# Optimization experiments

Measured on AMD Instinct MI355X. Metric: run time of the kernel, lower is better.

Reference implementation:

```python
import jax, jax.numpy as jnp
import numpy as np

NUM_GRAPHS = 128
EPS = 1e-5  # torch BatchNorm1d default eps


def setup_inputs() -> dict:
    key = jax.random.key(0)
    ks = jax.random.split(key, 24)
    N, E, NHE = 50000, 800000, 50000
    NODE_RAW, HEDGE_RAW, H, HH, HOUT = 92, 40, 128, 128, 256
    s = 0.05
    inp = {
        "x": jax.random.normal(ks[0], (N, NODE_RAW), jnp.float32),
        "hedge_attrs": jax.random.normal(ks[1], (NHE, HEDGE_RAW), jnp.float32),
        "inter_relations_index": jax.random.randint(ks[2], (3, E), 0, N, jnp.int64),
        "batch": jax.random.randint(ks[3], (N,), 0, NUM_GRAPHS, jnp.int64),
        "num_nodes": N,
        # embed: Linear(92, h_dim)
        "embed_w": jax.random.normal(ks[4], (NODE_RAW, H), jnp.float32) * s,
        "embed_b": jax.random.normal(ks[5], (H,), jnp.float32) * s,
        # bembed: Linear(hedge_dim, hidden_hedge_dim)
        "bembed_w": jax.random.normal(ks[6], (HEDGE_RAW, HH), jnp.float32) * s,
        "bembed_b": jax.random.normal(ks[7], (HH,), jnp.float32) * s,
        # conv.lin_full_presplit: Linear(2H+HH, 2H)
        "lin_w": jax.random.normal(ks[8], (2 * H + HH, 2 * H), jnp.float32) * s,
        "lin_b": jax.random.normal(ks[9], (2 * H,), jnp.float32) * s,
        "bn1_g": jnp.ones((2 * H,), jnp.float32),
        "bn1_b": jnp.zeros((2 * H,), jnp.float32),
        "bn2_g": jnp.ones((H,), jnp.float32),
        "bn2_b": jnp.zeros((H,), jnp.float32),
        # learnable temperature of SoftmaxAggregation (init 1.0)
        "aggr_t": jnp.ones((), jnp.float32),
        "l1_w": jax.random.normal(ks[10], (H, HOUT), jnp.float32) * s,
        "l1_b": jax.random.normal(ks[11], (HOUT,), jnp.float32) * s,
        "out_w": jax.random.normal(ks[12], (HOUT, 1), jnp.float32) * s,
        "out_b": jax.random.normal(ks[13], (1,), jnp.float32) * s,
    }
    return inp


def _batchnorm(z, g, b):
    mu = z.mean(axis=0)
    var = z.var(axis=0)  # biased, matching torch training-mode normalization
    return (z - mu) * jax.lax.rsqrt(var + EPS) * g + b


def reference(x, hedge_attrs, inter_relations_index, batch, num_nodes,
              embed_w, embed_b, bembed_w, bembed_b, lin_w, lin_b,
              bn1_g, bn1_b, bn2_g, bn2_b, aggr_t, l1_w, l1_b, out_w, out_b):
    idx0 = inter_relations_index[0]
    idx1 = inter_relations_index[1]
    connect_feats = hedge_attrs @ bembed_w + bembed_b          # [NHE, HH]
    h = x @ embed_w + embed_b                                   # [N, H]

    # --- CHGInterConv ---
    origin = h[idx0]                                            # [E, H]
    connect = connect_feats[idx1]                               # [E, HH]
    remote = h[idx0]                                            # faithful to source (uses idx0)
    z = jnp.concatenate([origin, connect, remote], axis=1)      # [E, 2H+HH]
    z = z @ lin_w + lin_b                                       # [E, 2H]
    z = _batchnorm(z, bn1_g, bn1_b)
    z_f, z_c = jnp.split(z, 2, axis=-1)
    msg = jax.nn.sigmoid(z_f) * jax.nn.softplus(z_c)            # [E, H]

    # learned SoftmaxAggregation: per-node, per-channel segment softmax of t*msg
    alpha = msg * aggr_t
    m = jax.ops.segment_max(alpha, idx0, num_segments=num_nodes)
    m = jnp.where(jnp.isfinite(m), m, 0.0)                      # empty segments
    e = jnp.exp(alpha - m[idx0])
    denom = jax.ops.segment_sum(e, idx0, num_segments=num_nodes)
    w = e / (denom[idx0] + 1e-16)
    out = jax.ops.segment_sum(msg * w, idx0, num_segments=num_nodes)  # [N, H]

    out = _batchnorm(out, bn2_g, bn2_b)
    h = jax.nn.softplus(out + h)                                # residual + softplus

    # --- global mean pool over graphs ---
    counts = jax.ops.segment_sum(jnp.ones((num_nodes,), h.dtype), batch,
                                 num_segments=NUM_GRAPHS)
    pooled = jax.ops.segment_sum(h, batch, num_segments=NUM_GRAPHS)
    pooled = pooled / jnp.maximum(counts, 1.0)[:, None]         # [G, H]

    g = jax.nn.softplus(pooled @ l1_w + l1_b)                   # [G, HOUT]
    return g @ out_w + out_b                                    # [G, 1]
```

## Files before the change

### kernel.cpp

```cpp
#include <hip/hip_runtime.h>
#include <hip/hip_bf16.h>


#define EPS_BN 1e-5f
#define LOG2E 1.4426950408889634f
#define LN2   0.6931471805599453f

#define BIN_SH 8
#define BIN_CHUNK 4096

typedef __attribute__((ext_vector_type(8))) short bf16x8;
typedef __attribute__((ext_vector_type(4))) float f32x4;
typedef __attribute__((ext_vector_type(2))) float f32x2;

__device__ __forceinline__ float fexp2(float x) {
#if __has_builtin(__builtin_amdgcn_exp2f)
    return __builtin_amdgcn_exp2f(x);
#else
    return __expf(x * LN2);
#endif
}
__device__ __forceinline__ float flog2(float x) {
#if __has_builtin(__builtin_amdgcn_logf)
    return __builtin_amdgcn_logf(x);
#else
    return __logf(x) * LOG2E;
#endif
}
__device__ __forceinline__ float softplus_fast(float x) {
    return LN2 * flog2(1.f + fexp2(x * LOG2E));
}

__device__ __forceinline__ f32x2 pk_fma2(f32x2 a, f32x2 b, f32x2 c) {
#if __has_builtin(__builtin_elementwise_fma)
    return __builtin_elementwise_fma(a, b, c);
#else
    return (f32x2){fmaf(a.x, b.x, c.x), fmaf(a.y, b.y, c.y)};
#endif
}

__device__ __forceinline__ unsigned short f2bf(float f) {
    unsigned u = __float_as_uint(f);
    unsigned r = (u + 0x7fffu + ((u >> 16) & 1u)) >> 16;
    return (unsigned short)r;
}
__device__ __forceinline__ float bflo(unsigned u) { return __uint_as_float(u << 16); }
__device__ __forceinline__ float bfhi(unsigned u) { return __uint_as_float(u & 0xffff0000u); }
__device__ __forceinline__ float bfu16(unsigned short v) { return __uint_as_float(((unsigned)v) << 16); }
__device__ __forceinline__ unsigned pack2bf(float x, float y) {
    return (unsigned)f2bf(x) | ((unsigned)f2bf(y) << 16);
}

#if __has_builtin(__builtin_amdgcn_cvt_pk_f32_fp8) && __has_builtin(__builtin_amdgcn_cvt_pk_fp8_f32)
#define HW_FP8 1
#else
#define HW_FP8 0
#endif

__device__ __forceinline__ unsigned char f2fp8(float f) {
#if HW_FP8
    int r = __builtin_amdgcn_cvt_pk_fp8_f32(f, f, 0, false);
    return (unsigned char)(r & 0xff);
#else
    unsigned u = __float_as_uint(f);
    unsigned s = (u >> 24) & 0x80u;
    float af = fabsf(f);
    if (!(af >= 0.015625f)) {
        int m = (int)rintf(af * 512.f);
        if (m > 7) m = 7;
        return (unsigned char)(s | (unsigned)m);
    }
    if (af > 448.f) return (unsigned char)(s | 0x7e);
    unsigned au = __float_as_uint(af);
    unsigned r = au + 0x7ffffu + ((au >> 20) & 1u);
    int e8 = (int)(r >> 23) - 120;
    unsigned m = (r >> 20) & 7u;
    if (e8 > 15 || (e8 == 15 && m == 7)) return (unsigned char)(s | 0x7e);
    return (unsigned char)(s | ((unsigned)e8 << 3) | m);
#endif
}

__device__ __forceinline__ void fp8pair(unsigned p, f32x2& lo, f32x2& hi) {
#if HW_FP8
    lo = __builtin_amdgcn_cvt_pk_f32_fp8((int)p, false);
    hi = __builtin_amdgcn_cvt_pk_f32_fp8((int)p, true);
#else
    auto dec = [](unsigned byte) -> float {
        unsigned s = (byte & 0x80u) << 24;
        unsigned em = byte & 0x7fu;
        float nrm = __uint_as_float(s | ((em << 20) + 0x3C000000u));
        float sub = __uint_as_float(s | 0x3F800000u) * (float)em * 0.001953125f;
        return (em >= 8) ? nrm : sub;
    };
    lo = (f32x2){dec(p & 0xff), dec((p >> 8) & 0xff)};
    hi = (f32x2){dec((p >> 16) & 0xff), dec(p >> 24)};
#endif
}

__device__ __forceinline__ int perm256(int j) {
    return (j < 128) ? ((j >> 1) * 4 + (j & 1)) : (((j - 128) >> 1) * 4 + 2 + (j & 1));
}

__global__ __launch_bounds__(256) void k_prepw(const float* __restrict__ ew, const float* __restrict__ bw,
                                               const float* __restrict__ lw,
                                               unsigned short* __restrict__ embB, unsigned short* __restrict__ bembB,
                                               unsigned short* __restrict__ waB, unsigned short* __restrict__ wcB) {
    int i = blockIdx.x * 256 + threadIdx.x;
    if (i >= 81920) return;
    unsigned short* dst;
    int f, NKC, CT, mode;
    if (i < 12288)      { dst = embB;  f = i;         NKC = 3; CT = 2; mode = 0; }
    else if (i < 20480) { dst = bembB; f = i - 12288; NKC = 2; CT = 2; mode = 1; }
    else if (i < 53248) { dst = waB;   f = i - 20480; NKC = 4; CT = 4; mode = 2; }
    else                { dst = wcB;   f = i - 53248; NKC = 4; CT = 4; mode = 3; }
    int j = f & 7, l = (f >> 3) & 63;
    int r2 = f >> 9;
    int c = r2 % CT;
    int r3 = r2 / CT;
    int kc = r3 % NKC, w = r3 / NKC;
    int k = kc * 32 + ((l >> 4) & 3) * 8 + j;
    int n = (w * CT + c) * 16 + (l & 15);
    float v;
    if (mode == 0)      v = (k < 92) ? ew[k * 128 + n] : 0.f;
    else if (mode == 1) v = (k < 40) ? bw[k * 128 + n] : 0.f;
    else if (mode == 2) v = lw[k * 256 + n] + lw[(k + 256) * 256 + n];
    else                v = lw[(k + 128) * 256 + n];
    dst[f] = f2bf(v);
}

template<int KIN, int NKC1, int OMODE2>
__global__ __launch_bounds__(256) void mfma_fused(
    const float* __restrict__ in, const unsigned short* __restrict__ B1, const float* __restrict__ bias1,
    const unsigned short* __restrict__ B2, const float* __restrict__ bias2,
    unsigned short* __restrict__ hout, void* __restrict__ out2, int M,
    const int* __restrict__ aux_idx, int* __restrict__ aux_hist, int aux_cnt)
{
    const int r0 = blockIdx.x * 32;
    const int t = threadIdx.x;
    const int w = t >> 6;
    const int l = t & 63;
    const int m = l & 15, q = l >> 4;

    if (aux_idx) {
        const int T = gridDim.x * 256;
        for (int i = blockIdx.x * 256 + t; i < aux_cnt; i += T)
            atomicAdd(&aux_hist[aux_idx[i]], 1);
    }

    __shared__ __align__(16) unsigned short als[32 * NKC1 * 32];
    __shared__ __align__(16) unsigned short hls[32 * 136];

    const int KP = NKC1 * 32;
    for (int i = t; i < 32 * KP; i += 256) {
        int r = i / KP, k = i - r * KP;
        int gr = r0 + r;
        float v = (gr < M && k < KIN) ? in[(size_t)gr * KIN + k] : 0.f;
        int idx = (((r >> 4) * NKC1 + (k >> 5)) * 64 + ((k >> 3) & 3) * 16 + (r & 15)) * 8 + (k & 7);
        als[idx] = f2bf(v);
    }
    bf16x8 b1[NKC1][2];
    const bf16x8* B1f = (const bf16x8*)B1;
#pragma unroll
    for (int kc = 0; kc < NKC1; kc++)
#pragma unroll
        for (int c = 0; c < 2; c++)
            b1[kc][c] = B1f[((w * NKC1 + kc) * 2 + c) * 64 + l];
    __syncthreads();

    f32x4 acc1[2][2];
#pragma unroll
    for (int c = 0; c < 2; c++) { acc1[c][0] = (f32x4){0.f,0.f,0.f,0.f}; acc1[c][1] = (f32x4){0.f,0.f,0.f,0.f}; }
    const bf16x8* af = (const bf16x8*)als;
#pragma unroll
    for (int kc = 0; kc < NKC1; kc++) {
        bf16x8 a0 = af[kc * 64 + l];
        bf16x8 a1 = af[(NKC1 + kc) * 64 + l];
#pragma unroll
        for (int c = 0; c < 2; c++) {
            acc1[c][0] = __builtin_amdgcn_mfma_f32_16x16x32_bf16(a0, b1[kc][c], acc1[c][0], 0, 0, 0);
            acc1[c][1] = __builtin_amdgcn_mfma_f32_16x16x32_bf16(a1, b1[kc][c], acc1[c][1], 0, 0, 0);
        }
    }
#pragma unroll
    for (int c = 0; c < 2; c++) {
        int n1 = (w * 2 + c) * 16 + m;
        float bv = bias1[n1];
#pragma unroll
        for (int hh = 0; hh < 2; hh++) {
#pragma unroll
            for (int r = 0; r < 4; r++) {
                int row = hh * 16 + q * 4 + r;
                float val = acc1[c][hh][r] + bv;
                unsigned short bf = f2bf(val);
                hls[row * 136 + n1] = bf;
                if (OMODE2 == 1 && r0 + row < M) hout[(size_t)(r0 + row) * 128 + n1] = bf;
            }
        }
    }
    __syncthreads();

    bf16x8 b2[4][4];
    const bf16x8* B2f = (const bf16x8*)B2;
#pragma unroll
    for (int kc = 0; kc < 4; kc++)
#pragma unroll
        for (int c = 0; c < 4; c++)
            b2[kc][c] = B2f[((w * 4 + kc) * 4 + c) * 64 + l];

    f32x4 acc2[4][2];
#pragma unroll
    for (int c = 0; c < 4; c++) { acc2[c][0] = (f32x4){0.f,0.f,0.f,0.f}; acc2[c][1] = (f32x4){0.f,0.f,0.f,0.f}; }
#pragma unroll
    for (int kc = 0; kc < 4; kc++) {
        bf16x8 a0 = *(const bf16x8*)(hls + m * 136 + kc * 32 + q * 8);
        bf16x8 a1 = *(const bf16x8*)(hls + (m + 16) * 136 + kc * 32 + q * 8);
#pragma unroll
        for (int c = 0; c < 4; c++) {
            acc2[c][0] = __builtin_amdgcn_mfma_f32_16x16x32_bf16(a0, b2[kc][c], acc2[c][0], 0, 0, 0);
            acc2[c][1] = __builtin_amdgcn_mfma_f32_16x16x32_bf16(a1, b2[kc][c], acc2[c][1], 0, 0, 0);
        }
    }
#pragma unroll
    for (int c = 0; c < 4; c++) {
        int n = (w * 4 + c) * 16 + m;
        float bv = bias2 ? bias2[n] : 0.f;
        int pj = perm256(n);
#pragma unroll
        for (int hh = 0; hh < 2; hh++) {
#pragma unroll
            for (int r = 0; r < 4; r++) {
                int row = r0 + hh * 16 + q * 4 + r;
                if (row < M) {
                    float val = acc2[c][hh][r] + bv;
                    if (OMODE2 == 1) ((unsigned short*)out2)[(size_t)row * 256 + pj] = f2bf(val);
                    else             ((unsigned char*)out2)[(size_t)row * 256 + pj] = f2fp8(val);
                }
            }
        }
    }
}

__global__ __launch_bounds__(256) void k_scanA(const int* __restrict__ hist, int* __restrict__ rloc,
                                               int* __restrict__ bsum, int N) {
    __shared__ int s[256];
    const int t = threadIdx.x;
    const int n0 = blockIdx.x << 8;
    const int nn = min(N - n0, 256);
    int v = (t < nn) ? hist[n0 + t] : 0;
    s[t] = v;
    __syncthreads();
#pragma unroll
    for (int ofs = 1; ofs < 256; ofs <<= 1) {
        int u = (t >= ofs) ? s[t - ofs] : 0;
        __syncthreads();
        s[t] += u;
        __syncthreads();
    }
    if (t < nn) rloc[n0 + t] = s[t] - v;
    if (t == 255) bsum[blockIdx.x] = s[255];
}

__global__ __launch_bounds__(256) void k_scanB(const int* __restrict__ bsum, int* __restrict__ boff,
                                               const int* __restrict__ gcount, int* __restrict__ gptr, int NB) {
    __shared__ int s[256];
    const int t = threadIdx.x;
    int v = (t < NB) ? bsum[t] : 0;
    s[t] = v;
    __syncthreads();
#pragma unroll
    for (int ofs = 1; ofs < 256; ofs <<= 1) {
        int u = (t >= ofs) ? s[t - ofs] : 0;
        __syncthreads();
        s[t] += u;
        __syncthreads();
    }
    if (t < NB) boff[t] = s[t] - v;
    if (t == NB - 1) boff[NB] = s[t];
    __syncthreads();
    int gv = (t < 128) ? gcount[t] : 0;
    s[t] = gv;
    __syncthreads();
#pragma unroll
    for (int ofs = 1; ofs < 128; ofs <<= 1) {
        int u = (t >= ofs && t < 128) ? s[t - ofs] : 0;
        __syncthreads();
        if (t < 128) s[t] += u;
        __syncthreads();
    }
    if (t < 128) gptr[t + 1] = s[t];
    if (t == 0) gptr[0] = 0;
}

__global__ __launch_bounds__(256) void k_binA(
    const int* __restrict__ idx0, const int* __restrict__ idx1,
    const int* __restrict__ boff, const int* __restrict__ rloc,
    int* __restrict__ rowptr, int* __restrict__ bfill,
    int* __restrict__ staging,
    const int* __restrict__ batch, const int* __restrict__ gptr,
    int* __restrict__ gfill, int* __restrict__ gnodes,
    int2* __restrict__ slots,
    int E, int N, int NB, int EB, int GB, int per_slot, int nslots)
{
    const int t = threadIdx.x;
    const int bid = blockIdx.x;
    if (bid >= EB + GB + NB) {
        int s = (bid - EB - GB - NB) * 256 + t;
        if (s > nslots) return;
        long base = (long)s * per_slot;
        if (base >= E) { slots[s] = (int2){N, N - 1}; return; }
        int e0 = (int)base;
        auto rp = [&](int n) { return boff[n >> BIN_SH] + rloc[n]; };
        int lo = 0, hi = N;
        while (lo + 1 < hi) { int mid = (lo + hi) >> 1; if (rp(mid) <= e0) lo = mid; else hi = mid; }
        int nS = lo;
        int nA = 0;
        if (e0 > 0) {
            lo = 0; hi = N;
            while (lo + 1 < hi) { int mid = (lo + hi) >> 1; if (rp(mid) < e0) lo = mid; else hi = mid; }
            nA = hi;
        }
        slots[s] = (int2){nA, nS};
        return;
    }
    if (bid >= EB + GB) {
        int i = ((bid - EB - GB) << 8) + t;
        if (i < N) rowptr[i] = boff[i >> BIN_SH] + rloc[i];
        if (bid == EB + GB && t == 0) rowptr[N] = boff[NB];
        return;
    }
    if (bid >= EB) {
        int i = (bid - EB) * 256 + t;
        if (i < N) {
            int g = batch[i];
            int pos = gptr[g] + atomicAdd(&gfill[g], 1);
            gnodes[pos] = i;
        }
        return;
    }
    __shared__ int svals[BIN_CHUNK];
    __shared__ unsigned char sbk[BIN_CHUNK];
    __shared__ int lhist[256], lbase[256];
    const int e0 = bid * BIN_CHUNK;
    const int cnt = min(E - e0, BIN_CHUNK);
    for (int b = t; b < NB; b += 256) lhist[b] = 0;
    __syncthreads();
    for (int i = t; i < cnt; i += 256) {
        int n = idx0[e0 + i];
        int m = idx1[e0 + i];
        int bk = n >> BIN_SH;
        sbk[i] = (unsigned char)bk;
        svals[i] = (m << BIN_SH) | (n & ((1 << BIN_SH) - 1));
        atomicAdd(&lhist[bk], 1);
    }
    __syncthreads();
    for (int b = t; b < NB; b += 256) {
        int h = lhist[b];
        int base = h ? atomicAdd(&bfill[b], h) : 0;
        lbase[b] = boff[b] + base;
        lhist[b] = 0;
    }
    __syncthreads();
    for (int i = t; i < cnt; i += 256) {
        int bk = sbk[i];
        int r = atomicAdd(&lhist[bk], 1);
        staging[lbase[bk] + r] = svals[i];
    }
}

__global__ __launch_bounds__(256) void k_binB(
    const int* __restrict__ rowptr, const int* __restrict__ staging,
    int* __restrict__ sidx1, int N)
{
    __shared__ int rp[257];
    __shared__ int lcnt[256];
    const int t = threadIdx.x;
    const int n0 = blockIdx.x << BIN_SH;
    const int nn = min(N - n0, 256);
    for (int j = t; j <= nn; j += 256) rp[j] = rowptr[n0 + j];
    lcnt[t] = 0;
    __syncthreads();
    const int s0 = rp[0], s1 = rp[nn];
    for (int i = s0 + t; i < s1; i += 256) {
        int v = staging[i];
        int nl = v & 255;
        int r = atomicAdd(&lcnt[nl], 1);
        sidx1[rp[nl] + r] = v & 0xffffff00;
    }
}

__global__ __launch_bounds__(256) void k_stats(const uint2* __restrict__ A16, const unsigned char* __restrict__ Cp8b,
                                               const int* __restrict__ rowptr, const int* __restrict__ sidx1,
                                               const int2* __restrict__ slots,
                                               float* __restrict__ gsum, float* __restrict__ gsq,
                                               int E, int N, int per_slot) {
    __shared__ float4 lsm4[256], lsq4[256];
    const int t = threadIdx.x;
    const int l = t & 63;
    const int wid = __builtin_amdgcn_readfirstlane(t >> 6);
    const int slot = blockIdx.x * 4 + wid;
    const unsigned lo4 = (unsigned)(l << 2);
    const long base = (long)slot * per_slot;
    const int e0 = (int)min((long)E, base);
    const int e1 = (int)min((long)E, base + per_slot);
    f32x2 smF = {0.f,0.f}, smC = {0.f,0.f};
    f32x2 sqF = {0.f,0.f}, sqC = {0.f,0.f};
    f32x2 csrF = {0.f,0.f}, csrC = {0.f,0.f};
    f32x2 aF = {0.f,0.f}, aC = {0.f,0.f};
    int cur_n = 0, bound = 0, runk = 0;

    auto flush = [&]() {
        if (runk) {
            float fk = (float)runk;
            f32x2 fk2 = {fk, fk};
            smF += csrF; smC += csrC;
            smF = pk_fma2(fk2, aF, smF);
            smC = pk_fma2(fk2, aC, smC);
            f32x2 tF = pk_fma2(fk2, aF, csrF + csrF);
            f32x2 tC = pk_fma2(fk2, aC, csrC + csrC);
            sqF = pk_fma2(aF, tF, sqF);
            sqC = pk_fma2(aC, tC, sqC);
        }
        csrF = (f32x2){0.f,0.f}; csrC = (f32x2){0.f,0.f};
        runk = 0;
    };
    auto loadA = [&](int n) {
        uint2 a8 = A16[(size_t)n * 64 + l];
        aF = (f32x2){bflo(a8.x), bfhi(a8.x)};
        aC = (f32x2){bflo(a8.y), bfhi(a8.y)};
    };

    if (e0 < e1) {
        cur_n = __builtin_amdgcn_readfirstlane(slots[slot].y);
        bound = __builtin_amdgcn_readfirstlane(rowptr[cur_n + 1]);
        loadA(cur_n);
    }

    auto proc = [&](int e, unsigned p) {
        if (e >= bound) {
            flush();
            do { cur_n++; bound = __builtin_amdgcn_readfirstlane(rowptr[cur_n + 1]); } while (bound <= e);
            loadA(cur_n);
        }
        f32x2 vf, vc;
        fp8pair(p, vf, vc);
        csrF += vf; csrC += vc;
        sqF = pk_fma2(vf, vf, sqF);
        sqC = pk_fma2(vc, vc, sqC);
        runk++;
    };

    const int nfull = (e1 - e0) & ~7;
    if (nfull > 0) {
        int eg = e0;
        unsigned cur[8];
        {
            int4 m0 = *(const int4*)(sidx1 + eg);
            int4 m1 = *(const int4*)(sidx1 + eg + 4);
            cur[0] = *(const unsigned*)(Cp8b + ((unsigned)m0.x + lo4));
            cur[1] = *(const unsigned*)(Cp8b + ((unsigned)m0.y + lo4));
            cur[2] = *(const unsigned*)(Cp8b + ((unsigned)m0.z + lo4));
            cur[3] = *(const unsigned*)(Cp8b + ((unsigned)m0.w + lo4));
            cur[4] = *(const unsigned*)(Cp8b + ((unsigned)m1.x + lo4));
            cur[5] = *(const unsigned*)(Cp8b + ((unsigned)m1.y + lo4));
            cur[6] = *(const unsigned*)(Cp8b + ((unsigned)m1.z + lo4));
            cur[7] = *(const unsigned*)(Cp8b + ((unsigned)m1.w + lo4));
        }
        for (;;) {
            const int en = eg + 8;
            const bool more = en < e0 + nfull;
            unsigned nxt[8];
            if (more) {
                int4 t0 = *(const int4*)(sidx1 + en);
                int4 t1 = *(const int4*)(sidx1 + en + 4);
                nxt[0] = *(const unsigned*)(Cp8b + ((unsigned)t0.x + lo4));
                nxt[1] = *(const unsigned*)(Cp8b + ((unsigned)t0.y + lo4));
                nxt[2] = *(const unsigned*)(Cp8b + ((unsigned)t0.z + lo4));
                nxt[3] = *(const unsigned*)(Cp8b + ((unsigned)t0.w + lo4));
                nxt[4] = *(const unsigned*)(Cp8b + ((unsigned)t1.x + lo4));
                nxt[5] = *(const unsigned*)(Cp8b + ((unsigned)t1.y + lo4));
                nxt[6] = *(const unsigned*)(Cp8b + ((unsigned)t1.z + lo4));
                nxt[7] = *(const unsigned*)(Cp8b + ((unsigned)t1.w + lo4));
            }
            proc(eg, cur[0]);     proc(eg + 1, cur[1]);
            proc(eg + 2, cur[2]); proc(eg + 3, cur[3]);
            proc(eg + 4, cur[4]); proc(eg + 5, cur[5]);
            proc(eg + 6, cur[6]); proc(eg + 7, cur[7]);
            if (!more) break;
#pragma unroll
            for (int i = 0; i < 8; i++) cur[i] = nxt[i];
            eg = en;
        }
    }
    for (int e = e0 + nfull; e < e1; e++)
        proc(e, *(const unsigned*)(Cp8b + ((unsigned)sidx1[e] + lo4)));
    flush();

    lsm4[t] = (float4){smF.x, smF.y, smC.x, smC.y};
    lsq4[t] = (float4){sqF.x, sqF.y, sqC.x, sqC.y};
    __syncthreads();
    const float* fm = (const float*)lsm4;
    const float* fq = (const float*)lsq4;
    float vs = fm[t] + fm[256 + t] + fm[512 + t] + fm[768 + t];
    float vq = fq[t] + fq[256 + t] + fq[512 + t] + fq[768 + t];
    atomicAdd(&gsum[t], vs);
    atomicAdd(&gsq[t], vq);
}

__global__ __launch_bounds__(256) void k_aggr(const uint2* __restrict__ A16, const unsigned char* __restrict__ Cp8b,
                                              const int* __restrict__ rowptr, const int* __restrict__ sidx1,
                                              const float* __restrict__ bn1_sum, const float* __restrict__ bn1_sq,
                                              const float* __restrict__ g1, const float* __restrict__ b1,
                                              const float* __restrict__ tptr, unsigned* __restrict__ out,
                                              float invE, int N) {
    const int t = threadIdx.x;
    const int l = t & 63;
    const int wid = __builtin_amdgcn_readfirstlane(t >> 6);
    const int n = blockIdx.x * 4 + wid;
    if (n >= N) return;

    const int e0 = __builtin_amdgcn_readfirstlane(rowptr[n]);
    const int e1 = __builtin_amdgcn_readfirstlane(rowptr[n + 1]);

    const float tt = tptr[0];
    const float4 sum4 = ((const float4*)bn1_sum)[l];
    const float4 sq4  = ((const float4*)bn1_sq)[l];
    const float2 gf = ((const float2*)g1)[l];
    const float2 gc = ((const float2*)(g1 + 128))[l];
    const float2 bf2 = ((const float2*)b1)[l];
    const float2 bc2 = ((const float2*)(b1 + 128))[l];
    auto mkss = [&](float sum, float sq, float gg, float bb, float& sc, float& sh) {
        float mu = sum * invE;
        float var = sq * invE - mu * mu;
        sc = gg * rsqrtf(var + EPS_BN);
        sh = fmaf(-mu, sc, bb);
    };
    float scx, shx, scy, shy, scz, shz, scw, shw;
    mkss(sum4.x, sq4.x, gf.x, bf2.x, scx, shx);
    mkss(sum4.y, sq4.y, gf.y, bf2.y, scy, shy);
    mkss(sum4.z, sq4.z, gc.x, bc2.x, scz, shz);
    mkss(sum4.w, sq4.w, gc.y, bc2.y, scw, shw);
    const f32x2 sF  = {-scx * LOG2E, -scy * LOG2E};
    const f32x2 sC  = { scz * LOG2E,  scw * LOG2E};

    uint2 a8 = A16[(size_t)n * 64 + l];
    f32x2 aF = {bflo(a8.x), bfhi(a8.x)}, aC = {bflo(a8.y), bfhi(a8.y)};
    const f32x2 bF = pk_fma2(aF, sF, (f32x2){-shx * LOG2E, -shy * LOG2E});
    const f32x2 bC = pk_fma2(aC, sC, (f32x2){ shz * LOG2E,  shw * LOG2E});

    if (e0 >= e1) { out[(size_t)n * 64 + l] = 0u; return; }

    const unsigned lo4 = (unsigned)(l << 2);
    f32x2 den = {0.f,0.f}, num = {0.f,0.f};

    auto G = [&](int e) -> unsigned {
        return *(const unsigned*)(Cp8b + ((unsigned)sidx1[e] + lo4));
    };
    auto procg = [&](unsigned p) {
        f32x2 vf, vc;
        fp8pair(p, vf, vc);
        f32x2 argf = pk_fma2(vf, sF, bF);
        f32x2 argc = pk_fma2(vc, sC, bC);
        f32x2 ef = {fexp2(argf.x), fexp2(argf.y)};
        f32x2 uu = {fexp2(argc.x), fexp2(argc.y)};
        f32x2 d1 = ef + 1.f;
        f32x2 u1 = uu + 1.f;
        f32x2 sig = {__builtin_amdgcn_rcpf(d1.x), __builtin_amdgcn_rcpf(d1.y)};
        f32x2 lg = {flog2(u1.x), flog2(u1.y)};
        f32x2 M = sig * lg;
        f32x2 tM = M * tt;
        f32x2 w = {fexp2(tM.x), fexp2(tM.y)};
        den += w;
        num = pk_fma2(M, w, num);
    };

    const int cnt = e1 - e0;
    unsigned cur[8];
#pragma unroll
    for (int i = 0; i < 8; i++)
        if (i < cnt) cur[i] = G(e0 + i);

    int e = e0;
    while (e + 8 < e1) {
        unsigned nxt[8];
#pragma unroll
        for (int i = 0; i < 8; i++)
            if (e + 8 + i < e1) nxt[i] = G(e + 8 + i);
#pragma unroll
        for (int i = 0; i < 8; i++) procg(cur[i]);
#pragma unroll
        for (int i = 0; i < 8; i++) cur[i] = nxt[i];
        e += 8;
    }
    const int rem = e1 - e;
#pragma unroll
    for (int i = 0; i < 8; i++)
        if (i < rem) procg(cur[i]);

    float ox = LN2 * num.x * __builtin_amdgcn_rcpf(den.x);
    float oy = LN2 * num.y * __builtin_amdgcn_rcpf(den.y);
    out[(size_t)n * 64 + l] = pack2bf(ox, oy);
}

__global__ __launch_bounds__(256) void k_bn2stats(const unsigned* __restrict__ outw, float* __restrict__ sum,
                                                  float* __restrict__ sq, int N) {
    __shared__ float4 ls[256];
    const int t = threadIdx.x;
    const int w = t & 63;
    const int rg = t >> 6;
    f32x2 sm = {0.f,0.f}, s2 = {0.f,0.f};
    for (int n = blockIdx.x * 4 + rg; n < N; n += gridDim.x * 4) {
        unsigned v = outw[(size_t)n * 64 + w];
        f32x2 x = {bflo(v), bfhi(v)};
        sm += x;
        s2 = pk_fma2(x, x, s2);
    }
    ls[t] = (float4){sm.x, sm.y, s2.x, s2.y};
    __syncthreads();
    if (t < 64) {
        float4 a = ls[t], b = ls[t + 64], c = ls[t + 128], d = ls[t + 192];
        atomicAdd(&sum[2 * w],     a.x + b.x + c.x + d.x);
        atomicAdd(&sum[2 * w + 1], a.y + b.y + c.y + d.y);
        atomicAdd(&sq[2 * w],      a.z + b.z + c.z + d.z);
        atomicAdd(&sq[2 * w + 1],  a.w + b.w + c.w + d.w);
    }
}

template<int SPLIT>
__global__ __launch_bounds__(128) void k_h2pool(const unsigned short* __restrict__ out,
                                                const unsigned short* __restrict__ h,
                                                const int* __restrict__ gptr, const int* __restrict__ gnodes,
                                                const float* __restrict__ bn2_sum, const float* __restrict__ bn2_sq,
                                                const float* __restrict__ g2, const float* __restrict__ b2,
                                                float* __restrict__ pooled, float invN) {
    const int g = blockIdx.x & 127;
    const int sp = blockIdx.x >> 7;
    const int c = threadIdx.x;
    float mu = bn2_sum[c] * invN;
    float var = bn2_sq[c] * invN - mu * mu;
    float sc = g2[c] * rsqrtf(var + EPS_BN);
    float sh = fmaf(-mu, sc, b2[c]);
    const int i0 = gptr[g], i1 = gptr[g + 1];
    float acc = 0.f;
    for (int i = i0 + sp; i < i1; i += SPLIT) {
        int n = gnodes[i];
        float v = fmaf(bfu16(out[(size_t)n * 128 + c]), sc, sh) + bfu16(h[(size_t)n * 128 + c]);
        acc += softplus_fast(v);
    }
    if (acc != 0.f) atomicAdd(&pooled[g * 128 + c], acc);
}

__global__ __launch_bounds__(256) void k_head(const float* __restrict__ pooled, const int* __restrict__ gcount,
                                              const float* __restrict__ l1w, const float* __restrict__ l1b,
                                              const float* __restrict__ outw, const float* __restrict__ outb,
                                              float* __restrict__ dout) {
    __shared__ float p[128];
    __shared__ float red[256];
    const int g = blockIdx.x;
    const int j = threadIdx.x;
    if (j < 128) {
        float cnt = (float)max(gcount[g], 1);
        p[j] = pooled[g * 128 + j] / cnt;
    }
    __syncthreads();
    float acc = l1b[j];
    for (int k = 0; k < 128; k++) acc = fmaf(p[k], l1w[k * 256 + j], acc);
    red[j] = softplus_fast(acc) * outw[j];
    __syncthreads();
    for (int s = 128; s > 0; s >>= 1) {
        if (j < s) red[j] += red[j + s];
        __syncthreads();
    }
    if (j == 0) dout[g] = red[0] + outb[0];
}

extern "C" void kernel_launch(void* const* d_in, const int* in_sizes, int n_in,
                              void* d_out, int out_size, void* d_ws, size_t ws_size,
                              hipStream_t stream) {
    const float* x        = (const float*)d_in[0];
    const float* hedge    = (const float*)d_in[1];
    const int*   iri      = (const int*)d_in[2];
    const int*   batch    = (const int*)d_in[3];
    const float* embed_w  = (const float*)d_in[5];
    const float* embed_b  = (const float*)d_in[6];
    const float* bembed_w = (const float*)d_in[7];
    const float* bembed_b = (const float*)d_in[8];
    const float* lin_w    = (const float*)d_in[9];
    const float* lin_b    = (const float*)d_in[10];
    const float* bn1_g    = (const float*)d_in[11];
    const float* bn1_b    = (const float*)d_in[12];
    const float* bn2_g    = (const float*)d_in[13];
    const float* bn2_b    = (const float*)d_in[14];
    const float* aggr_t   = (const float*)d_in[15];
    const float* l1_w     = (const float*)d_in[16];
    const float* l1_b     = (const float*)d_in[17];
    const float* out_w    = (const float*)d_in[18];
    const float* out_b    = (const float*)d_in[19];

    const int N   = in_sizes[0] / 92;
    const int NHE = in_sizes[1] / 40;
    const int E   = in_sizes[2] / 3;
    const int* idx0 = iri;
    const int* idx1 = iri + E;

    float* ws = (float*)d_ws;
    size_t off = 0;
    auto alloc = [&](size_t elems) -> float* {
        float* p = ws + off;
        off += (elems + 63) & ~(size_t)63;
        return p;
    };
    unsigned short* h16 = (unsigned short*)alloc((size_t)N * 64);
    uint2* A16    = (uint2*)alloc((size_t)N * 128);
    unsigned* Cp8 = (unsigned*)alloc((size_t)NHE * 64);
    unsigned short* embB  = (unsigned short*)alloc(6144);
    unsigned short* bembB = (unsigned short*)alloc(4096);
    unsigned short* waB   = (unsigned short*)alloc(16384);
    unsigned short* wcB   = (unsigned short*)alloc(16384);
    int*   rowptr = (int*)alloc((size_t)N + 1);
    int*   rloc   = (int*)alloc((size_t)N);
    int*   bsum   = (int*)alloc(256);
    int*   boff   = (int*)alloc(260);
    int*   sidx1  = (int*)alloc((size_t)E + 8);
    int*   staging = (int*)alloc((size_t)E + 8);
    int*   gptr   = (int*)alloc(129);
    int*   gnodes = (int*)alloc((size_t)N);
    unsigned* outbuf = (unsigned*)alloc((size_t)N * 64);
    int2*  slots  = (int2*)alloc(2 * 8200);
    float* zbase  = ws + off;
    int*   hist   = (int*)alloc((size_t)N);
    int*   bfill  = (int*)alloc(256);
    int*   gfill  = (int*)alloc(128);
    float* bn1_sum = alloc(256);
    float* bn1_sq  = alloc(256);
    float* bn2_sum = alloc(128);
    float* bn2_sq  = alloc(128);
    float* pooled  = alloc(128 * 128);
    int*   gcount  = (int*)alloc(128);
    size_t zbytes = (size_t)((ws + off) - zbase) * sizeof(float);
    (void)ws_size;

    hipMemsetAsync(zbase, 0, zbytes, stream);

    k_prepw<<<320, 256, 0, stream>>>(embed_w, bembed_w, lin_w, embB, bembB, waB, wcB);
    const int mtN   = (N + 31) / 32;
    const int mtNHE = (NHE + 31) / 32;
    mfma_fused<92, 3, 1><<<mtN, 256, 0, stream>>>(x, embB, embed_b, waB, lin_b, h16, A16, N,
                                                  idx0, hist, E);
    mfma_fused<40, 2, 2><<<mtNHE, 256, 0, stream>>>(hedge, bembB, bembed_b, wcB, nullptr, nullptr, Cp8, NHE,
                                                    batch, gcount, N);

    const int NB = (N + 255) >> BIN_SH;
    k_scanA<<<NB, 256, 0, stream>>>(hist, rloc, bsum, N);
    k_scanB<<<1, 256, 0, stream>>>(bsum, boff, gcount, gptr, NB);

    const int EDGE_BLOCKS = 2048;
    const int NSLOTS = EDGE_BLOCKS * 4;
    int per_slot = ((E + NSLOTS - 1) / NSLOTS + 7) & ~7;
    int nslots_used = (E + per_slot - 1) / per_slot;

    const int EB = (E + BIN_CHUNK - 1) / BIN_CHUNK;
    const int GB = (N + 255) / 256;
    const int SL_BLOCKS = (nslots_used + 1 + 255) / 256;
    k_binA<<<EB + GB + NB + SL_BLOCKS, 256, 0, stream>>>(
        idx0, idx1, boff, rloc, rowptr, bfill, staging,
        batch, gptr, gfill, gnodes, slots, E, N, NB, EB, GB, per_slot, nslots_used);

    k_binB<<<NB, 256, 0, stream>>>(rowptr, staging, sidx1, N);

    k_stats<<<EDGE_BLOCKS, 256, 0, stream>>>(A16, (const unsigned char*)Cp8, rowptr, sidx1, slots,
                                             bn1_sum, bn1_sq, E, N, per_slot);

    k_aggr<<<(N + 3) / 4, 256, 0, stream>>>(A16, (const unsigned char*)Cp8, rowptr, sidx1,
                                            bn1_sum, bn1_sq, bn1_g, bn1_b, aggr_t, outbuf,
                                            1.0f / (float)E, N);

    k_bn2stats<<<256, 256, 0, stream>>>((const unsigned*)outbuf, bn2_sum, bn2_sq, N);
    k_h2pool<16><<<128 * 16, 128, 0, stream>>>((const unsigned short*)outbuf, h16, gptr, gnodes,
                                               bn2_sum, bn2_sq, bn2_g, bn2_b, pooled, 1.0f / (float)N);

    k_head<<<128, 256, 0, stream>>>(pooled, gcount, l1_w, l1_b, out_w, out_b, (float*)d_out);
}
```

Baseline: 466.9 us.

## Build CSR via per-bucket counts instead of per-node histogram scan

Replaces the per-node degree histogram (built inside the embedding GEMM with global atomics) plus per-node scan with a coarse per-bucket count kernel using shared-memory atomics. Per-node row offsets are now computed inside k_binB by a local histogram and scan over each bucket's staged edges. The precomputed slot table is dropped and each k_stats wave binary-searches rowptr itself. The aim is fewer global atomics and fewer launched blocks, at the cost of an extra pass over idx0 and the staging array and per-wave scalar binary searches.

```diff
diff --git a/kernel.cpp b/kernel.cpp
--- a/kernel.cpp
+++ b/kernel.cpp
@@ -240,24 +240,18 @@
     }
 }
 
-__global__ __launch_bounds__(256) void k_scanA(const int* __restrict__ hist, int* __restrict__ rloc,
-                                               int* __restrict__ bsum, int N) {
-    __shared__ int s[256];
+__global__ __launch_bounds__(256) void k_count(const int* __restrict__ idx0, int* __restrict__ bsum,
+                                               int E, int NB) {
+    __shared__ int lhist[256];
     const int t = threadIdx.x;
-    const int n0 = blockIdx.x << 8;
-    const int nn = min(N - n0, 256);
-    int v = (t < nn) ? hist[n0 + t] : 0;
-    s[t] = v;
-    __syncthreads();
-#pragma unroll
-    for (int ofs = 1; ofs < 256; ofs <<= 1) {
-        int u = (t >= ofs) ? s[t - ofs] : 0;
-        __syncthreads();
-        s[t] += u;
-        __syncthreads();
-    }
-    if (t < nn) rloc[n0 + t] = s[t] - v;
-    if (t == 255) bsum[blockIdx.x] = s[255];
+    const int e0 = blockIdx.x * BIN_CHUNK;
+    const int cnt = min(E - e0, BIN_CHUNK);
+    lhist[t] = 0;
+    __syncthreads();
+    for (int i = t; i < cnt; i += 256)
+        atomicAdd(&lhist[idx0[e0 + i] >> BIN_SH], 1);
+    __syncthreads();
+    if (t < NB && lhist[t]) atomicAdd(&bsum[t], lhist[t]);
 }
 
 __global__ __launch_bounds__(256) void k_scanB(const int* __restrict__ bsum, int* __restrict__ boff,
@@ -293,41 +287,14 @@
 
 __global__ __launch_bounds__(256) void k_binA(
     const int* __restrict__ idx0, const int* __restrict__ idx1,
-    const int* __restrict__ boff, const int* __restrict__ rloc,
-    int* __restrict__ rowptr, int* __restrict__ bfill,
+    const int* __restrict__ boff, int* __restrict__ bfill,
     int* __restrict__ staging,
     const int* __restrict__ batch, const int* __restrict__ gptr,
     int* __restrict__ gfill, int* __restrict__ gnodes,
-    int2* __restrict__ slots,
-    int E, int N, int NB, int EB, int GB, int per_slot, int nslots)
+    int E, int N, int NB, int EB)
 {
     const int t = threadIdx.x;
     const int bid = blockIdx.x;
-    if (bid >= EB + GB + NB) {
-        int s = (bid - EB - GB - NB) * 256 + t;
-        if (s > nslots) return;
-        long base = (long)s * per_slot;
-        if (base >= E) { slots[s] = (int2){N, N - 1}; return; }
-        int e0 = (int)base;
-        auto rp = [&](int n) { return boff[n >> BIN_SH] + rloc[n]; };
-        int lo = 0, hi = N;
-        while (lo + 1 < hi) { int mid = (lo + hi) >> 1; if (rp(mid) <= e0) lo = mid; else hi = mid; }
-        int nS = lo;
-        int nA = 0;
-        if (e0 > 0) {
-            lo = 0; hi = N;
-            while (lo + 1 < hi) { int mid = (lo + hi) >> 1; if (rp(mid) < e0) lo = mid; else hi = mid; }
-            nA = hi;
-        }
-        slots[s] = (int2){nA, nS};
-        return;
-    }
-    if (bid >= EB + GB) {
-        int i = ((bid - EB - GB) << 8) + t;
-        if (i < N) rowptr[i] = boff[i >> BIN_SH] + rloc[i];
-        if (bid == EB + GB && t == 0) rowptr[N] = boff[NB];
-        return;
-    }
     if (bid >= EB) {
         int i = (bid - EB) * 256 + t;
         if (i < N) {
@@ -368,29 +335,47 @@
 }
 
 __global__ __launch_bounds__(256) void k_binB(
-    const int* __restrict__ rowptr, const int* __restrict__ staging,
-    int* __restrict__ sidx1, int N)
+    const int* __restrict__ boff, const int* __restrict__ staging,
+    int* __restrict__ rowptr, int* __restrict__ sidx1, int E, int N)
 {
-    __shared__ int rp[257];
     __shared__ int lcnt[256];
+    __shared__ int noofs[256];
+    __shared__ int s[256];
     const int t = threadIdx.x;
-    const int n0 = blockIdx.x << BIN_SH;
+    const int b = blockIdx.x;
+    const int n0 = b << BIN_SH;
     const int nn = min(N - n0, 256);
-    for (int j = t; j <= nn; j += 256) rp[j] = rowptr[n0 + j];
+    const int s0 = boff[b], s1 = boff[b + 1];
     lcnt[t] = 0;
     __syncthreads();
-    const int s0 = rp[0], s1 = rp[nn];
+    for (int i = s0 + t; i < s1; i += 256)
+        atomicAdd(&lcnt[staging[i] & 255], 1);
+    __syncthreads();
+    int v = lcnt[t];
+    s[t] = v;
+    __syncthreads();
+#pragma unroll
+    for (int ofs = 1; ofs < 256; ofs <<= 1) {
+        int u = (t >= ofs) ? s[t - ofs] : 0;
+        __syncthreads();
+        s[t] += u;
+        __syncthreads();
+    }
+    noofs[t] = s[t] - v;
+    if (t < nn) rowptr[n0 + t] = s0 + s[t] - v;
+    lcnt[t] = 0;
+    if (b == 0 && t == 0) rowptr[N] = E;
+    __syncthreads();
     for (int i = s0 + t; i < s1; i += 256) {
-        int v = staging[i];
-        int nl = v & 255;
+        int vv = staging[i];
+        int nl = vv & 255;
         int r = atomicAdd(&lcnt[nl], 1);
-        sidx1[rp[nl] + r] = v & 0xffffff00;
+        sidx1[s0 + noofs[nl] + r] = vv & 0xffffff00;
     }
 }
 
 __global__ __launch_bounds__(256) void k_stats(const uint2* __restrict__ A16, const unsigned char* __restrict__ Cp8b,
                                                const int* __restrict__ rowptr, const int* __restrict__ sidx1,
-                                               const int2* __restrict__ slots,
                                                float* __restrict__ gsum, float* __restrict__ gsq,
                                                int E, int N, int per_slot) {
     __shared__ float4 lsm4[256], lsq4[256];
@@ -430,7 +415,13 @@
     };
 
     if (e0 < e1) {
-        cur_n = __builtin_amdgcn_readfirstlane(slots[slot].y);
+        int lo = 0, hi = N;
+        while (lo + 1 < hi) {
+            int mid = (lo + hi) >> 1;
+            int rv = __builtin_amdgcn_readfirstlane(rowptr[mid]);
+            if (rv <= e0) lo = mid; else hi = mid;
+        }
+        cur_n = lo;
         bound = __builtin_amdgcn_readfirstlane(rowptr[cur_n + 1]);
         loadA(cur_n);
     }
@@ -717,17 +708,14 @@
     unsigned short* waB   = (unsigned short*)alloc(16384);
     unsigned short* wcB   = (unsigned short*)alloc(16384);
     int*   rowptr = (int*)alloc((size_t)N + 1);
-    int*   rloc   = (int*)alloc((size_t)N);
-    int*   bsum   = (int*)alloc(256);
     int*   boff   = (int*)alloc(260);
     int*   sidx1  = (int*)alloc((size_t)E + 8);
     int*   staging = (int*)alloc((size_t)E + 8);
     int*   gptr   = (int*)alloc(129);
     int*   gnodes = (int*)alloc((size_t)N);
     unsigned* outbuf = (unsigned*)alloc((size_t)N * 64);
-    int2*  slots  = (int2*)alloc(2 * 8200);
     float* zbase  = ws + off;
-    int*   hist   = (int*)alloc((size_t)N);
+    int*   bsum   = (int*)alloc(256);
     int*   bfill  = (int*)alloc(256);
     int*   gfill  = (int*)alloc(128);
     float* bn1_sum = alloc(256);
@@ -745,29 +733,25 @@
     const int mtN   = (N + 31) / 32;
     const int mtNHE = (NHE + 31) / 32;
     mfma_fused<92, 3, 1><<<mtN, 256, 0, stream>>>(x, embB, embed_b, waB, lin_b, h16, A16, N,
-                                                  idx0, hist, E);
+                                                  nullptr, nullptr, 0);
     mfma_fused<40, 2, 2><<<mtNHE, 256, 0, stream>>>(hedge, bembB, bembed_b, wcB, nullptr, nullptr, Cp8, NHE,
                                                     batch, gcount, N);
 
     const int NB = (N + 255) >> BIN_SH;
-    k_scanA<<<NB, 256, 0, stream>>>(hist, rloc, bsum, N);
+    const int EB = (E + BIN_CHUNK - 1) / BIN_CHUNK;
+    k_count<<<EB, 256, 0, stream>>>(idx0, bsum, E, NB);
     k_scanB<<<1, 256, 0, stream>>>(bsum, boff, gcount, gptr, NB);
+
+    const int GB = (N + 255) / 256;
+    k_binA<<<EB + GB, 256, 0, stream>>>(idx0, idx1, boff, bfill, staging,
+                                        batch, gptr, gfill, gnodes, E, N, NB, EB);
+
+    k_binB<<<NB, 256, 0, stream>>>(boff, staging, rowptr, sidx1, E, N);
 
     const int EDGE_BLOCKS = 2048;
     const int NSLOTS = EDGE_BLOCKS * 4;
     int per_slot = ((E + NSLOTS - 1) / NSLOTS + 7) & ~7;
-    int nslots_used = (E + per_slot - 1) / per_slot;
-
-    const int EB = (E + BIN_CHUNK - 1) / BIN_CHUNK;
-    const int GB = (N + 255) / 256;
-    const int SL_BLOCKS = (nslots_used + 1 + 255) / 256;
-    k_binA<<<EB + GB + NB + SL_BLOCKS, 256, 0, stream>>>(
-        idx0, idx1, boff, rloc, rowptr, bfill, staging,
-        batch, gptr, gfill, gnodes, slots, E, N, NB, EB, GB, per_slot, nslots_used);
-
-    k_binB<<<NB, 256, 0, stream>>>(rowptr, staging, sidx1, N);
-
-    k_stats<<<EDGE_BLOCKS, 256, 0, stream>>>(A16, (const unsigned char*)Cp8, rowptr, sidx1, slots,
+    k_stats<<<EDGE_BLOCKS, 256, 0, stream>>>(A16, (const unsigned char*)Cp8, rowptr, sidx1,
                                              bn1_sum, bn1_sq, E, N, per_slot);
 
     k_aggr<<<(N + 3) / 4, 256, 0, stream>>>(A16, (const unsigned char*)Cp8, rowptr, sidx1,
```

New measurement: 444.8 us. 1.05x faster.
